# Optimization experiments

Hardware: AMD Instinct MI355X
Metric: run time of the kernel (lower is better)

The kernel has to match this reference:

```python
import jax, jax.numpy as jnp
import numpy as np
from jax import lax

SCORE_THRESH = 0.05
NMS_THRESH = 0.5
TOPK = 100
NEG = -1.0  # scores are softmax probs in (0,1); -1 acts as -inf for sorting/top-k


def _iou_matrix(b):
    # b: (R,4) xyxy -> (R,R) pairwise IoU (torchvision convention, no +1)
    area = (b[:, 2] - b[:, 0]) * (b[:, 3] - b[:, 1])
    lt = jnp.maximum(b[:, None, :2], b[None, :, :2])
    rb = jnp.minimum(b[:, None, 2:], b[None, :, 2:])
    wh = jnp.clip(rb - lt, 0.0)
    inter = wh[..., 0] * wh[..., 1]
    union = area[:, None] + area[None, :] - inter
    return inter / jnp.maximum(union, 1e-9)


def _nms_one_class(b_c, s_c):
    # b_c: (R,4), s_c: (R,). Greedy NMS in descending-score order.
    order = jnp.argsort(-s_c)
    b = b_c[order]
    s = s_c[order]
    valid = s > SCORE_THRESH
    iou = _iou_matrix(b)  # (R,R)
    R = b.shape[0]

    def body(i, state):
        keep, active = state
        ki = active[i] & valid[i]
        keep = keep.at[i].set(ki)
        active = active & ~(ki & (iou[i] > NMS_THRESH))
        return keep, active

    keep, _ = lax.fori_loop(0, R, body,
                            (jnp.zeros(R, bool), jnp.ones(R, bool)))
    return b, jnp.where(keep, s, NEG)


def setup_inputs() -> dict:
    key = jax.random.key(0)
    k1, k2, k3, k4, k5 = jax.random.split(key, 5)
    R, K = 1000, 80
    H, W = 800, 1333
    # Well-formed per-class boxes (x1<x2, y1<y2) roughly inside the image.
    cx = jax.random.uniform(k1, (R, K)) * W
    cy = jax.random.uniform(k2, (R, K)) * H
    w = jax.random.uniform(k3, (R, K)) * 200.0 + 10.0
    h = jax.random.uniform(k4, (R, K)) * 200.0 + 10.0
    boxes = jnp.stack([cx - w / 2, cy - h / 2, cx + w / 2, cy + h / 2],
                      axis=-1).reshape(R, K * 4).astype(jnp.float32)
    scores = jax.nn.softmax(jax.random.normal(k5, (R, K + 1)) * 2.0, axis=-1)
    return {"boxes": boxes, "scores": scores.astype(jnp.float32),
            "im_h": H, "im_w": W}


def reference(boxes, scores, im_h, im_w):
    R = boxes.shape[0]
    s = scores[:, :-1]            # (R,K) drop background column
    K = s.shape[1]
    b = boxes.reshape(R, K, 4)
    # clip to image (x in [0,W], y in [0,H])
    x = jnp.clip(b[..., 0::2], 0.0, float(im_w))
    y = jnp.clip(b[..., 1::2], 0.0, float(im_h))
    b = jnp.stack([x[..., 0], y[..., 0], x[..., 1], y[..., 1]], axis=-1)
    # per-class batched NMS, vmapped over the K class axis
    bb, ss = jax.vmap(_nms_one_class, in_axes=(1, 1))(b, s)  # (K,R,4),(K,R)
    classes = jnp.broadcast_to(jnp.arange(K, dtype=jnp.int32)[:, None], ss.shape)
    # global top-k over all surviving (class, box) candidates
    top_s, top_i = lax.top_k(ss.reshape(-1), TOPK)
    top_b = bb.reshape(-1, 4)[top_i]
    top_c = classes.reshape(-1)[top_i]
    dets = jnp.concatenate([top_b, top_s[:, None]], axis=-1)  # (TOPK,5)
    return dets, top_c
```

## Files before the change

kernel.cpp:

```cpp
#include <hip/hip_runtime.h>
#include <hip/hip_bf16.h>

#define R      1000
#define K      80
#define KP1    81
#define CAND   100
#define NC     (K*CAND)
#define VCAP   256
#define SCORE_THRESH 0.05f
#define NMS_THRESH   0.5f

typedef unsigned long long u64;

__device__ unsigned g_ctr = 0;

__device__ __forceinline__ unsigned int ordf(float f) {
    unsigned int u = __float_as_uint(f);
    return (u & 0x80000000u) ? ~u : (u | 0x80000000u);
}
__device__ __forceinline__ float unordf(unsigned int o) {
    unsigned int u = (o & 0x80000000u) ? (o ^ 0x80000000u) : ~o;
    return __uint_as_float(u);
}

__device__ __forceinline__ void st_agent_u64(u64* p, u64 v) {
    __hip_atomic_store(p, v, __ATOMIC_RELAXED, __HIP_MEMORY_SCOPE_AGENT);
}
__device__ __forceinline__ u64 ld_agent_u64(const u64* p) {
    return __hip_atomic_load(p, __ATOMIC_RELAXED, __HIP_MEMORY_SCOPE_AGENT);
}
__device__ __forceinline__ void st_box(float4* p, float4 b) {
    union { float f[2]; u64 u; } lo, hi;
    lo.f[0] = b.x; lo.f[1] = b.y; hi.f[0] = b.z; hi.f[1] = b.w;
    st_agent_u64((u64*)p, lo.u);
    st_agent_u64((u64*)p + 1, hi.u);
}
__device__ __forceinline__ float4 ld_box(const float4* p) {
    union { float f[2]; u64 u; } lo, hi;
    lo.u = ld_agent_u64((const u64*)p);
    hi.u = ld_agent_u64((const u64*)p + 1);
    return make_float4(lo.f[0], lo.f[1], hi.f[0], hi.f[1]);
}

template<int NR>
__device__ __forceinline__ void build_matrix(
    int lane, int w, int V, const float4* sboxs, u64* mat)
{
    float4 bx[NR]; float area[NR];
    #pragma unroll
    for (int r = 0; r < NR; ++r) {
        float4 bb = sboxs[r * 64 + lane];
        bx[r] = bb;
        area[r] = (bb.z - bb.x) * (bb.w - bb.y);
    }
    const int Vq = (V + 3) >> 2;
    int jbeg = w * Vq;
    int jend = jbeg + Vq; if (jend > V) jend = V;
    #pragma unroll 2
    for (int j = jbeg; j < jend; ++j) {
        float4 bj = sboxs[j];
        float areaB = (bj.z - bj.x) * (bj.w - bj.y);
        #pragma unroll
        for (int r = 0; r < NR; ++r) {
            float ltx = fmaxf(bx[r].x, bj.x), lty = fmaxf(bx[r].y, bj.y);
            float rbx = fminf(bx[r].z, bj.z), rby = fminf(bx[r].w, bj.w);
            float ww = fmaxf(rbx - ltx, 0.f), hh = fmaxf(rby - lty, 0.f);
            float inter = ww * hh;
            float uni = area[r] + areaB - inter;
            float iou = inter / fmaxf(uni, 1e-9f);
            mat[j * NR + r] = __ballot(iou > NMS_THRESH);
        }
    }
}

template<int NR>
__device__ __forceinline__ void scan_emit(
    int k, int lane, int V,
    const float4* sboxs, const float* sscs, const u64* mat,
    u64* __restrict__ cand_key, float4* __restrict__ cand_box)
{
    const u64 lt_mask = (1ull << lane) - 1ull;

    u64 kept[NR];
    #pragma unroll
    for (int r = 0; r < NR; ++r) kept[r] = 0ull;
    u64 cur[NR];
    #pragma unroll
    for (int r = 0; r < NR; ++r) cur[r] = mat[r];

    int j = 0;
    #pragma unroll
    for (int jc = 0; jc < NR; ++jc) {
        int jmax = V - jc * 64;
        if (jmax > 64) jmax = 64;
        for (int jl = 0; jl < jmax; ++jl, ++j) {
            u64 nxt[NR];
            #pragma unroll
            for (int r = 0; r < NR; ++r) nxt[r] = mat[(j + 1) * NR + r];
            u64 hit = 0ull;
            #pragma unroll
            for (int r = 0; r < NR; ++r) hit |= cur[r] & kept[r];
            if (hit == 0ull) kept[jc] |= (1ull << jl);
            #pragma unroll
            for (int r = 0; r < NR; ++r) cur[r] = nxt[r];
        }
    }

    unsigned pre = 0;
    u64* ck = cand_key + (size_t)k * CAND;
    float4* cb = cand_box + (size_t)k * CAND;
    #pragma unroll
    for (int r = 0; r < NR; ++r) {
        u64 m = kept[r];
        bool mine = (m >> lane) & 1ull;
        unsigned rank = pre + (unsigned)__popcll(m & lt_mask);
        if (mine && rank < CAND) {
            unsigned c = (unsigned)(k * CAND + rank);
            float s = sscs[r * 64 + lane];
            st_agent_u64(&ck[rank], ((u64)ordf(s) << 32) | (u64)(0xFFFFFFFFu - c));
            st_box(&cb[rank], sboxs[r * 64 + lane]);
        }
        pre += (unsigned)__popcll(m);
    }
    unsigned T100 = pre < CAND ? pre : CAND;
    for (unsigned s2 = T100 + (unsigned)lane; s2 < CAND; s2 += 64)
        st_agent_u64(&ck[s2], 0ull);
}

__global__ __launch_bounds__(256, 1) void fused_kernel(
    const float* __restrict__ boxes, const float* __restrict__ scores,
    const int* __restrict__ imh, const int* __restrict__ imw,
    u64* __restrict__ cand_key, float4* __restrict__ cand_box,
    float* __restrict__ out)
{
    const int k = blockIdx.x, tid = threadIdx.x;
    const int lane = tid & 63, w = tid >> 6;

    __shared__ u64    skey[VCAP];
    __shared__ float4 sbox[VCAP];
    __shared__ float4 sboxs[VCAP];
    __shared__ float  sscs[VCAP];
    __shared__ u64    mat[(VCAP + 1) * 4];
    __shared__ unsigned cnt16[16];
    __shared__ int lastf;
    __shared__ unsigned h768[768];
    __shared__ unsigned hist[4][264];
    __shared__ unsigned wsum[4];
    __shared__ u64 Psh;
    __shared__ unsigned remsh, cntsh, nExtsh, Bsh;
    __shared__ int donesh;
    __shared__ u64 Wl[256];

    const float Wf = (float)(*imw), Hf = (float)(*imh);

    float sv[4];
    #pragma unroll
    for (int t = 0; t < 4; ++t) {
        int i = w * 256 + t * 64 + lane;
        sv[t] = (i < R) ? scores[i * KP1 + k] : -1.f;
    }
    bool val[4]; unsigned posl[4];
    #pragma unroll
    for (int t = 0; t < 4; ++t) {
        bool v = sv[t] > SCORE_THRESH;
        u64 m = __ballot(v);
        val[t] = v;
        posl[t] = (unsigned)__popcll(m & ((1ull << lane) - 1ull));
        if (lane == 0) cnt16[w * 4 + t] = (unsigned)__popcll(m);
    }
    float4 rb[4];
    #pragma unroll
    for (int t = 0; t < 4; ++t) {
        if (val[t]) {
            int i = w * 256 + t * 64 + lane;
            rb[t] = *(const float4*)(boxes + (size_t)i * (K * 4) + (size_t)k * 4);
        }
    }
    __syncthreads();

    unsigned base4[4] = {0, 0, 0, 0};
    unsigned total = 0;
    #pragma unroll
    for (int x = 0; x < 16; ++x) {
        unsigned cc = cnt16[x];
        #pragma unroll
        for (int t = 0; t < 4; ++t) if (x < w * 4 + t) base4[t] += cc;
        total += cc;
    }
    const int V = total < VCAP ? (int)total : VCAP;

    #pragma unroll
    for (int t = 0; t < 4; ++t) {
        if (val[t]) {
            unsigned pos = base4[t] + posl[t];
            if (pos < VCAP) {
                skey[pos] = ((u64)ordf(sv[t]) << 32) | (u64)(0xFFFFFFFFu - pos);
                float4 bb = rb[t];
                bb.x = fminf(fmaxf(bb.x, 0.f), Wf);
                bb.y = fminf(fmaxf(bb.y, 0.f), Hf);
                bb.z = fminf(fmaxf(bb.z, 0.f), Wf);
                bb.w = fminf(fmaxf(bb.w, 0.f), Hf);
                sbox[pos] = bb;
            }
        }
    }
    __syncthreads();

    if (tid < V) {
        u64 my = skey[tid];
        int rank = 0;
        #pragma unroll 4
        for (int j = 0; j < V; ++j) rank += (skey[j] > my) ? 1 : 0;
        sboxs[rank] = sbox[tid];
        sscs[rank]  = unordf((unsigned)(my >> 32));
    }
    __syncthreads();

    if (V > 0) {
        if (V <= 64)       build_matrix<1>(lane, w, V, sboxs, mat);
        else if (V <= 128) build_matrix<2>(lane, w, V, sboxs, mat);
        else               build_matrix<4>(lane, w, V, sboxs, mat);
    }
    __syncthreads();

    if (w == 0) {
        if (V == 0) {
            for (int s2 = lane; s2 < CAND; s2 += 64)
                st_agent_u64(&cand_key[(size_t)k * CAND + s2], 0ull);
        } else if (V <= 64)  scan_emit<1>(k, lane, V, sboxs, sscs, mat, cand_key, cand_box);
        else if (V <= 128)   scan_emit<2>(k, lane, V, sboxs, sscs, mat, cand_key, cand_box);
        else                 scan_emit<4>(k, lane, V, sboxs, sscs, mat, cand_key, cand_box);
    }
    __syncthreads();

    if (tid == 0) {
        unsigned old = __hip_atomic_fetch_add(&g_ctr, 1u, __ATOMIC_RELAXED, __HIP_MEMORY_SCOPE_AGENT);
        lastf = ((old % (unsigned)K) == (unsigned)(K - 1)) ? 1 : 0;
    }
    __syncthreads();
    if (!lastf) return;

    u64 keyv[32];
    #pragma unroll
    for (int j = 0; j < 32; ++j) {
        int idx = tid + 256 * j;
        keyv[j] = (idx < NC) ? ld_agent_u64(&cand_key[idx]) : 0ull;
    }

    #pragma unroll
    for (int x = 0; x < 3; ++x) h768[x * 256 + tid] = 0;
    __syncthreads();
    #pragma unroll
    for (int j = 0; j < 32; ++j) {
        u64 kk = keyv[j];
        if (kk != 0ull)
            atomicAdd(&h768[(unsigned)(kk >> 48) - 0xBD00u], 1u);
    }
    __syncthreads();

    {
        unsigned h0 = h768[3 * tid], h1 = h768[3 * tid + 1], h2 = h768[3 * tid + 2];
        unsigned local = h0 + h1 + h2;
        unsigned inc = local;
        #pragma unroll
        for (int off = 1; off < 64; off <<= 1) {
            unsigned v = __shfl_down(inc, off);
            if (lane + off < 64) inc += v;
        }
        if (lane == 0) wsum[w] = inc;
        __syncthreads();
        unsigned wafter = 0;
        #pragma unroll
        for (int ww = 0; ww < 4; ++ww) if (ww > w) wafter += wsum[ww];
        unsigned after = inc - local + wafter;

        unsigned G2 = after;
        unsigned G1 = after + h2;
        unsigned G0 = after + h2 + h1;
        if (h2 && G2 <= CAND - 1 && CAND - 1 < G2 + h2) {
            Bsh = 3 * tid + 2; remsh = CAND - 1 - G2; nExtsh = G2 + h2; cntsh = 0; donesh = 0;
        }
        if (h1 && G1 <= CAND - 1 && CAND - 1 < G1 + h1) {
            Bsh = 3 * tid + 1; remsh = CAND - 1 - G1; nExtsh = G1 + h1; cntsh = 0; donesh = 0;
        }
        if (h0 && G0 <= CAND - 1 && CAND - 1 < G0 + h0) {
            Bsh = 3 * tid;     remsh = CAND - 1 - G0; nExtsh = G0 + h0; cntsh = 0; donesh = 0;
        }
        __syncthreads();
    }

    const unsigned B16 = Bsh + 0xBD00u;

    if (nExtsh <= 256) {
        #pragma unroll
        for (int j = 0; j < 32; ++j) {
            u64 kk = keyv[j];
            if (kk != 0ull && (unsigned)(kk >> 48) >= B16) {
                unsigned pos = atomicAdd(&cntsh, 1u);
                Wl[pos] = kk;
            }
        }
        __syncthreads();
        const int n = (int)nExtsh;
        if (tid < n) {
            u64 my = Wl[tid];
            int r = 0;
            for (int j = 0; j < n; ++j) r += (Wl[j] > my) ? 1 : 0;
            if (r < CAND) {
                unsigned c = 0xFFFFFFFFu - (unsigned)my;
                float s = unordf((unsigned)(my >> 32));
                float4 bb = ld_box(&cand_box[c]);
                out[r * 5 + 0] = bb.x;
                out[r * 5 + 1] = bb.y;
                out[r * 5 + 2] = bb.z;
                out[r * 5 + 3] = bb.w;
                out[r * 5 + 4] = s;
                out[500 + r]   = (float)(c / CAND);
            }
        }
        return;
    }

    if (tid == 0) Psh = (u64)B16 << 48;
    __syncthreads();

    const int plist[4] = {5, 4, 1, 0};
    for (int pi = 0; pi < 4; ++pi) {
        if (donesh) break;
        const int p = plist[pi];
        const int shift = 8 * p;
        #pragma unroll
        for (int ww = 0; ww < 4; ++ww) hist[ww][tid] = 0;
        __syncthreads();

        u64 pfx = Psh;
        unsigned rem = remsh;
        u64 hmask = ~0ull << (shift + 8);
        #pragma unroll
        for (int j = 0; j < 32; ++j) {
            u64 kk = keyv[j];
            if (kk != 0ull && ((kk ^ pfx) & hmask) == 0ull)
                atomicAdd(&hist[w][(unsigned)(kk >> shift) & 0xFFu], 1u);
        }
        __syncthreads();

        int b = 255 - tid;
        unsigned v = hist[0][b] + hist[1][b] + hist[2][b] + hist[3][b];
        unsigned inc = v;
        #pragma unroll
        for (int off = 1; off < 64; off <<= 1) {
            unsigned t2 = __shfl_up(inc, off);
            if (lane >= off) inc += t2;
        }
        if (lane == 63) wsum[w] = inc;
        __syncthreads();
        unsigned woff = 0;
        #pragma unroll
        for (int ww = 0; ww < 4; ++ww) if (ww < w) woff += wsum[ww];
        inc += woff;
        unsigned cumG = inc - v;
        if (v > 0 && rem >= cumG && rem < cumG + v) {
            u64 np = Psh | ((u64)(unsigned)b << shift);
            if (p == 4) np |= 0xFFFF0000ull;
            unsigned rem_new = rem - cumG;
            Psh = np;
            remsh = rem_new;
            donesh = (v == rem_new + 1) ? 1 : 0;
        }
        __syncthreads();
    }

    const u64 T = Psh;
    #pragma unroll
    for (int j = 0; j < 32; ++j) {
        u64 kk = keyv[j];
        if (kk >= T && kk != 0ull) {
            unsigned pos = atomicAdd(&cntsh, 1u);
            if (pos < 256) Wl[pos] = kk;
        }
    }
    __syncthreads();

    if (tid < CAND) {
        u64 my = Wl[tid];
        int r = 0;
        for (int j = 0; j < CAND; ++j) r += (Wl[j] > my) ? 1 : 0;
        unsigned c = 0xFFFFFFFFu - (unsigned)my;
        float s = unordf((unsigned)(my >> 32));
        float4 bb = ld_box(&cand_box[c]);
        out[r * 5 + 0] = bb.x;
        out[r * 5 + 1] = bb.y;
        out[r * 5 + 2] = bb.z;
        out[r * 5 + 3] = bb.w;
        out[r * 5 + 4] = s;
        out[500 + r]   = (float)(c / CAND);
    }
}

extern "C" void kernel_launch(void* const* d_in, const int* in_sizes, int n_in,
                              void* d_out, int out_size, void* d_ws, size_t ws_size,
                              hipStream_t stream) {
    const float* boxes  = (const float*)d_in[0];
    const float* scores = (const float*)d_in[1];
    const int*   imh    = (const int*)d_in[2];
    const int*   imw    = (const int*)d_in[3];
    float* out = (float*)d_out;

    u64*    cand_key = (u64*)d_ws;
    float4* cand_box = (float4*)((char*)d_ws + 65536);

    fused_kernel<<<K, 256, 0, stream>>>(boxes, scores, imh, imw,
                                        cand_key, cand_box, out);
}
```

Before: 22.31 us.

## Add dedicated consumer block that streams per-class candidates via epoch flags

```diff
diff --git a/kernel.cpp b/kernel.cpp
--- a/kernel.cpp
+++ b/kernel.cpp
@@ -12,7 +12,8 @@
 
 typedef unsigned long long u64;
 
-__device__ unsigned g_ctr = 0;
+__device__ unsigned g_flags[K];
+__device__ unsigned g_cons = 0;
 
 __device__ __forceinline__ unsigned int ordf(float f) {
     unsigned int u = __float_as_uint(f);
@@ -133,7 +134,7 @@
     u64* __restrict__ cand_key, float4* __restrict__ cand_box,
     float* __restrict__ out)
 {
-    const int k = blockIdx.x, tid = threadIdx.x;
+    const int tid = threadIdx.x;
     const int lane = tid & 63, w = tid >> 6;
 
     __shared__ u64    skey[VCAP];
@@ -142,15 +143,185 @@
     __shared__ float  sscs[VCAP];
     __shared__ u64    mat[(VCAP + 1) * 4];
     __shared__ unsigned cnt16[16];
-    __shared__ int lastf;
     __shared__ unsigned h768[768];
     __shared__ unsigned hist[4][264];
     __shared__ unsigned wsum[4];
     __shared__ u64 Psh;
-    __shared__ unsigned remsh, cntsh, nExtsh, Bsh;
+    __shared__ unsigned remsh, cntsh, nExtsh, Bsh, Nsh;
     __shared__ int donesh;
     __shared__ u64 Wl[256];
 
+    if (blockIdx.x == K) {
+        if (tid == 0) {
+            unsigned old = __hip_atomic_fetch_add(&g_cons, 1u, __ATOMIC_RELAXED, __HIP_MEMORY_SCOPE_AGENT);
+            Nsh = old + 1u;
+            cntsh = 0;
+        }
+        #pragma unroll
+        for (int x = 0; x < 3; ++x) h768[x * 256 + tid] = 0;
+        __syncthreads();
+        const unsigned N = Nsh;
+
+        u64 ka[20], kb[20];
+        #pragma unroll
+        for (int i = 0; i < 20; ++i) {
+            const int k2 = w * 20 + i;
+            while (__hip_atomic_load(&g_flags[k2], __ATOMIC_RELAXED, __HIP_MEMORY_SCOPE_AGENT) < N)
+                __builtin_amdgcn_s_sleep(2);
+            asm volatile("" ::: "memory");
+            u64 a = ld_agent_u64(&cand_key[(size_t)k2 * CAND + lane]);
+            u64 b = (lane < CAND - 64) ? ld_agent_u64(&cand_key[(size_t)k2 * CAND + 64 + lane]) : 0ull;
+            ka[i] = a; kb[i] = b;
+            if (a) atomicAdd(&h768[(unsigned)(a >> 48) - 0xBD00u], 1u);
+            if (b) atomicAdd(&h768[(unsigned)(b >> 48) - 0xBD00u], 1u);
+        }
+        __syncthreads();
+
+        {
+            unsigned h0 = h768[3 * tid], h1 = h768[3 * tid + 1], h2 = h768[3 * tid + 2];
+            unsigned local = h0 + h1 + h2;
+            unsigned inc = local;
+            #pragma unroll
+            for (int off = 1; off < 64; off <<= 1) {
+                unsigned v = __shfl_down(inc, off);
+                if (lane + off < 64) inc += v;
+            }
+            if (lane == 0) wsum[w] = inc;
+            __syncthreads();
+            unsigned wafter = 0;
+            #pragma unroll
+            for (int ww = 0; ww < 4; ++ww) if (ww > w) wafter += wsum[ww];
+            unsigned after = inc - local + wafter;
+
+            unsigned G2 = after;
+            unsigned G1 = after + h2;
+            unsigned G0 = after + h2 + h1;
+            if (h2 && G2 <= CAND - 1 && CAND - 1 < G2 + h2) {
+                Bsh = 3 * tid + 2; remsh = CAND - 1 - G2; nExtsh = G2 + h2; donesh = 0;
+            }
+            if (h1 && G1 <= CAND - 1 && CAND - 1 < G1 + h1) {
+                Bsh = 3 * tid + 1; remsh = CAND - 1 - G1; nExtsh = G1 + h1; donesh = 0;
+            }
+            if (h0 && G0 <= CAND - 1 && CAND - 1 < G0 + h0) {
+                Bsh = 3 * tid;     remsh = CAND - 1 - G0; nExtsh = G0 + h0; donesh = 0;
+            }
+            __syncthreads();
+        }
+
+        const unsigned B16 = Bsh + 0xBD00u;
+
+        if (nExtsh <= 256) {
+            #pragma unroll
+            for (int i = 0; i < 20; ++i) {
+                u64 a = ka[i], b = kb[i];
+                if (a && (unsigned)(a >> 48) >= B16) { unsigned p = atomicAdd(&cntsh, 1u); Wl[p] = a; }
+                if (b && (unsigned)(b >> 48) >= B16) { unsigned p = atomicAdd(&cntsh, 1u); Wl[p] = b; }
+            }
+            __syncthreads();
+            const int n = (int)nExtsh;
+            if (tid < n) {
+                u64 my = Wl[tid];
+                int r = 0;
+                for (int j = 0; j < n; ++j) r += (Wl[j] > my) ? 1 : 0;
+                if (r < CAND) {
+                    unsigned c = 0xFFFFFFFFu - (unsigned)my;
+                    float s = unordf((unsigned)(my >> 32));
+                    float4 bb = ld_box(&cand_box[c]);
+                    out[r * 5 + 0] = bb.x;
+                    out[r * 5 + 1] = bb.y;
+                    out[r * 5 + 2] = bb.z;
+                    out[r * 5 + 3] = bb.w;
+                    out[r * 5 + 4] = s;
+                    out[500 + r]   = (float)(c / CAND);
+                }
+            }
+            return;
+        }
+
+        u64 keyv[32];
+        #pragma unroll
+        for (int j = 0; j < 32; ++j) {
+            int idx = tid + 256 * j;
+            keyv[j] = (idx < NC) ? ld_agent_u64(&cand_key[idx]) : 0ull;
+        }
+        if (tid == 0) Psh = (u64)B16 << 48;
+        __syncthreads();
+
+        const int plist[4] = {5, 4, 1, 0};
+        for (int pi = 0; pi < 4; ++pi) {
+            if (donesh) break;
+            const int p = plist[pi];
+            const int shift = 8 * p;
+            #pragma unroll
+            for (int ww = 0; ww < 4; ++ww) hist[ww][tid] = 0;
+            __syncthreads();
+
+            u64 pfx = Psh;
+            unsigned rem = remsh;
+            u64 hmask = ~0ull << (shift + 8);
+            #pragma unroll
+            for (int j = 0; j < 32; ++j) {
+                u64 kk = keyv[j];
+                if (kk != 0ull && ((kk ^ pfx) & hmask) == 0ull)
+                    atomicAdd(&hist[w][(unsigned)(kk >> shift) & 0xFFu], 1u);
+            }
+            __syncthreads();
+
+            int b = 255 - tid;
+            unsigned v = hist[0][b] + hist[1][b] + hist[2][b] + hist[3][b];
+            unsigned inc = v;
+            #pragma unroll
+            for (int off = 1; off < 64; off <<= 1) {
+                unsigned t2 = __shfl_up(inc, off);
+                if (lane >= off) inc += t2;
+            }
+            if (lane == 63) wsum[w] = inc;
+            __syncthreads();
+            unsigned woff = 0;
+            #pragma unroll
+            for (int ww = 0; ww < 4; ++ww) if (ww < w) woff += wsum[ww];
+            inc += woff;
+            unsigned cumG = inc - v;
+            if (v > 0 && rem >= cumG && rem < cumG + v) {
+                u64 np = Psh | ((u64)(unsigned)b << shift);
+                if (p == 4) np |= 0xFFFF0000ull;
+                unsigned rem_new = rem - cumG;
+                Psh = np;
+                remsh = rem_new;
+                donesh = (v == rem_new + 1) ? 1 : 0;
+            }
+            __syncthreads();
+        }
+
+        const u64 T = Psh;
+        #pragma unroll
+        for (int j = 0; j < 32; ++j) {
+            u64 kk = keyv[j];
+            if (kk >= T && kk != 0ull) {
+                unsigned pos = atomicAdd(&cntsh, 1u);
+                if (pos < 256) Wl[pos] = kk;
+            }
+        }
+        __syncthreads();
+
+        if (tid < CAND) {
+            u64 my = Wl[tid];
+            int r = 0;
+            for (int j = 0; j < CAND; ++j) r += (Wl[j] > my) ? 1 : 0;
+            unsigned c = 0xFFFFFFFFu - (unsigned)my;
+            float s = unordf((unsigned)(my >> 32));
+            float4 bb = ld_box(&cand_box[c]);
+            out[r * 5 + 0] = bb.x;
+            out[r * 5 + 1] = bb.y;
+            out[r * 5 + 2] = bb.z;
+            out[r * 5 + 3] = bb.w;
+            out[r * 5 + 4] = s;
+            out[500 + r]   = (float)(c / CAND);
+        }
+        return;
+    }
+
+    const int k = blockIdx.x;
     const float Wf = (float)(*imw), Hf = (float)(*imh);
 
     float sv[4];
@@ -230,170 +401,10 @@
         } else if (V <= 64)  scan_emit<1>(k, lane, V, sboxs, sscs, mat, cand_key, cand_box);
         else if (V <= 128)   scan_emit<2>(k, lane, V, sboxs, sscs, mat, cand_key, cand_box);
         else                 scan_emit<4>(k, lane, V, sboxs, sscs, mat, cand_key, cand_box);
-    }
-    __syncthreads();
-
-    if (tid == 0) {
-        unsigned old = __hip_atomic_fetch_add(&g_ctr, 1u, __ATOMIC_RELAXED, __HIP_MEMORY_SCOPE_AGENT);
-        lastf = ((old % (unsigned)K) == (unsigned)(K - 1)) ? 1 : 0;
-    }
-    __syncthreads();
-    if (!lastf) return;
-
-    u64 keyv[32];
-    #pragma unroll
-    for (int j = 0; j < 32; ++j) {
-        int idx = tid + 256 * j;
-        keyv[j] = (idx < NC) ? ld_agent_u64(&cand_key[idx]) : 0ull;
-    }
-
-    #pragma unroll
-    for (int x = 0; x < 3; ++x) h768[x * 256 + tid] = 0;
-    __syncthreads();
-    #pragma unroll
-    for (int j = 0; j < 32; ++j) {
-        u64 kk = keyv[j];
-        if (kk != 0ull)
-            atomicAdd(&h768[(unsigned)(kk >> 48) - 0xBD00u], 1u);
-    }
-    __syncthreads();
-
-    {
-        unsigned h0 = h768[3 * tid], h1 = h768[3 * tid + 1], h2 = h768[3 * tid + 2];
-        unsigned local = h0 + h1 + h2;
-        unsigned inc = local;
-        #pragma unroll
-        for (int off = 1; off < 64; off <<= 1) {
-            unsigned v = __shfl_down(inc, off);
-            if (lane + off < 64) inc += v;
-        }
-        if (lane == 0) wsum[w] = inc;
-        __syncthreads();
-        unsigned wafter = 0;
-        #pragma unroll
-        for (int ww = 0; ww < 4; ++ww) if (ww > w) wafter += wsum[ww];
-        unsigned after = inc - local + wafter;
-
-        unsigned G2 = after;
-        unsigned G1 = after + h2;
-        unsigned G0 = after + h2 + h1;
-        if (h2 && G2 <= CAND - 1 && CAND - 1 < G2 + h2) {
-            Bsh = 3 * tid + 2; remsh = CAND - 1 - G2; nExtsh = G2 + h2; cntsh = 0; donesh = 0;
-        }
-        if (h1 && G1 <= CAND - 1 && CAND - 1 < G1 + h1) {
-            Bsh = 3 * tid + 1; remsh = CAND - 1 - G1; nExtsh = G1 + h1; cntsh = 0; donesh = 0;
-        }
-        if (h0 && G0 <= CAND - 1 && CAND - 1 < G0 + h0) {
-            Bsh = 3 * tid;     remsh = CAND - 1 - G0; nExtsh = G0 + h0; cntsh = 0; donesh = 0;
-        }
-        __syncthreads();
-    }
-
-    const unsigned B16 = Bsh + 0xBD00u;
-
-    if (nExtsh <= 256) {
-        #pragma unroll
-        for (int j = 0; j < 32; ++j) {
-            u64 kk = keyv[j];
-            if (kk != 0ull && (unsigned)(kk >> 48) >= B16) {
-                unsigned pos = atomicAdd(&cntsh, 1u);
-                Wl[pos] = kk;
-            }
-        }
-        __syncthreads();
-        const int n = (int)nExtsh;
-        if (tid < n) {
-            u64 my = Wl[tid];
-            int r = 0;
-            for (int j = 0; j < n; ++j) r += (Wl[j] > my) ? 1 : 0;
-            if (r < CAND) {
-                unsigned c = 0xFFFFFFFFu - (unsigned)my;
-                float s = unordf((unsigned)(my >> 32));
-                float4 bb = ld_box(&cand_box[c]);
-                out[r * 5 + 0] = bb.x;
-                out[r * 5 + 1] = bb.y;
-                out[r * 5 + 2] = bb.z;
-                out[r * 5 + 3] = bb.w;
-                out[r * 5 + 4] = s;
-                out[500 + r]   = (float)(c / CAND);
-            }
-        }
-        return;
-    }
-
-    if (tid == 0) Psh = (u64)B16 << 48;
-    __syncthreads();
-
-    const int plist[4] = {5, 4, 1, 0};
-    for (int pi = 0; pi < 4; ++pi) {
-        if (donesh) break;
-        const int p = plist[pi];
-        const int shift = 8 * p;
-        #pragma unroll
-        for (int ww = 0; ww < 4; ++ww) hist[ww][tid] = 0;
-        __syncthreads();
-
-        u64 pfx = Psh;
-        unsigned rem = remsh;
-        u64 hmask = ~0ull << (shift + 8);
-        #pragma unroll
-        for (int j = 0; j < 32; ++j) {
-            u64 kk = keyv[j];
-            if (kk != 0ull && ((kk ^ pfx) & hmask) == 0ull)
-                atomicAdd(&hist[w][(unsigned)(kk >> shift) & 0xFFu], 1u);
-        }
-        __syncthreads();
-
-        int b = 255 - tid;
-        unsigned v = hist[0][b] + hist[1][b] + hist[2][b] + hist[3][b];
-        unsigned inc = v;
-        #pragma unroll
-        for (int off = 1; off < 64; off <<= 1) {
-            unsigned t2 = __shfl_up(inc, off);
-            if (lane >= off) inc += t2;
-        }
-        if (lane == 63) wsum[w] = inc;
-        __syncthreads();
-        unsigned woff = 0;
-        #pragma unroll
-        for (int ww = 0; ww < 4; ++ww) if (ww < w) woff += wsum[ww];
-        inc += woff;
-        unsigned cumG = inc - v;
-        if (v > 0 && rem >= cumG && rem < cumG + v) {
-            u64 np = Psh | ((u64)(unsigned)b << shift);
-            if (p == 4) np |= 0xFFFF0000ull;
-            unsigned rem_new = rem - cumG;
-            Psh = np;
-            remsh = rem_new;
-            donesh = (v == rem_new + 1) ? 1 : 0;
-        }
-        __syncthreads();
-    }
-
-    const u64 T = Psh;
-    #pragma unroll
-    for (int j = 0; j < 32; ++j) {
-        u64 kk = keyv[j];
-        if (kk >= T && kk != 0ull) {
-            unsigned pos = atomicAdd(&cntsh, 1u);
-            if (pos < 256) Wl[pos] = kk;
-        }
-    }
-    __syncthreads();
-
-    if (tid < CAND) {
-        u64 my = Wl[tid];
-        int r = 0;
-        for (int j = 0; j < CAND; ++j) r += (Wl[j] > my) ? 1 : 0;
-        unsigned c = 0xFFFFFFFFu - (unsigned)my;
-        float s = unordf((unsigned)(my >> 32));
-        float4 bb = ld_box(&cand_box[c]);
-        out[r * 5 + 0] = bb.x;
-        out[r * 5 + 1] = bb.y;
-        out[r * 5 + 2] = bb.z;
-        out[r * 5 + 3] = bb.w;
-        out[r * 5 + 4] = s;
-        out[500 + r]   = (float)(c / CAND);
+
+        asm volatile("s_waitcnt vmcnt(0)" ::: "memory");
+        if (lane == 0)
+            __hip_atomic_fetch_add(&g_flags[k], 1u, __ATOMIC_RELAXED, __HIP_MEMORY_SCOPE_AGENT);
     }
 }
 
@@ -409,6 +420,6 @@
     u64*    cand_key = (u64*)d_ws;
     float4* cand_box = (float4*)((char*)d_ws + 65536);
 
-    fused_kernel<<<K, 256, 0, stream>>>(boxes, scores, imh, imw,
-                                        cand_key, cand_box, out);
-}
+    fused_kernel<<<K + 1, 256, 0, stream>>>(boxes, scores, imh, imw,
+                                            cand_key, cand_box, out);
+}
```

Measured after the change: 31.39 us. 40.7% more time.
